# Kernel tuning notes

Hardware: AMD Instinct MI355X
Metric: run time of the kernel (lower is better)

## Reference

```python
import jax, jax.numpy as jnp
import numpy as np

T, H, I, E, TOPK = 2048, 2048, 1408, 8, 2


def setup_inputs() -> dict:
    key = jax.random.key(0)
    k1, k2, k3, k4 = jax.random.split(key, 4)
    x = jax.random.normal(k1, (T, H), dtype=jnp.float32)
    router_logits = jax.random.normal(k2, (T, E), dtype=jnp.float32)
    # scale weights down so activations stay well-conditioned
    w13_weight = jax.random.normal(k3, (E, 2 * I, H), dtype=jnp.float32) * (1.0 / np.sqrt(H))
    w2_weight = jax.random.normal(k4, (E, H, I), dtype=jnp.float32) * (1.0 / np.sqrt(I))
    return {"x": x, "router_logits": router_logits, "w13_weight": w13_weight,
            "w2_weight": w2_weight, "top_k": TOPK}


def reference(x, router_logits, w13_weight, w2_weight, top_k):
    # --- select_experts: softmax scoring, top-k, renormalize ---
    probs = jax.nn.softmax(router_logits.astype(jnp.float32), axis=-1)   # [T, E]
    topk_w, topk_ids = jax.lax.top_k(probs, top_k)                        # [T, k]
    topk_w = topk_w / jnp.sum(topk_w, axis=-1, keepdims=True)             # renormalize
    topk_w = topk_w.astype(x.dtype)

    n_tok = x.shape[0]
    n_exp = w13_weight.shape[0]
    inter = w2_weight.shape[2]

    # dense combine weights [T, E]: zero for unselected experts
    comb = jnp.zeros((n_tok, n_exp), dtype=x.dtype)
    comb = comb.at[jnp.arange(n_tok)[:, None], topk_ids].add(topk_w)

    # --- fused_experts: gated SiLU MLP per expert, weighted combine ---
    gate_up = jnp.einsum('th,eih->tei', x, w13_weight)                    # [T, E, 2I]
    gate, up = gate_up[..., :inter], gate_up[..., inter:]
    act = jax.nn.silu(gate) * up                                          # [T, E, I]
    out = jnp.einsum('tei,ehi,te->th', act, w2_weight, comb)              # [T, H]
    return out
```

## Files before the change

kernel.cpp:

```cpp
#include <hip/hip_runtime.h>
#include <hip/hip_bf16.h>
#include <stdint.h>

#define T_TOK 2048
#define H_DIM 2048
#define I_DIM 1408
#define NEXP  8
#define NPOS  4096
#define NPAD  5120
#define MAXT  40

typedef short short8 __attribute__((ext_vector_type(8)));
typedef float f32x4  __attribute__((ext_vector_type(4)));

__device__ __forceinline__ short f2bf(float f) {
  union { float f; uint32_t u; } v; v.f = f;
  uint32_t r = (v.u + 0x7FFFu + ((v.u >> 16) & 1u)) >> 16;
  return (short)r;
}

__device__ __forceinline__ short8 cvt8(f32x4 a, f32x4 b) {
  __hip_bfloat162 h0 = __float22bfloat162_rn(float2{a[0], a[1]});
  __hip_bfloat162 h1 = __float22bfloat162_rn(float2{a[2], a[3]});
  __hip_bfloat162 h2 = __float22bfloat162_rn(float2{b[0], b[1]});
  __hip_bfloat162 h3 = __float22bfloat162_rn(float2{b[2], b[3]});
  short2 s0, s1, s2, s3;
  __builtin_memcpy(&s0, &h0, 4); __builtin_memcpy(&s1, &h1, 4);
  __builtin_memcpy(&s2, &h2, 4); __builtin_memcpy(&s3, &h3, 4);
  short8 r;
  r[0] = s0.x; r[1] = s0.y; r[2] = s1.x; r[3] = s1.y;
  r[4] = s2.x; r[5] = s2.y; r[6] = s3.x; r[7] = s3.y;
  return r;
}

__device__ __forceinline__ void load_lds16(const void* g, void* l) {
  __builtin_amdgcn_global_load_lds((const __attribute__((address_space(1))) uint32_t*)g,
                                   (__attribute__((address_space(3))) uint32_t*)l,
                                   16, 0, 0);
}

__global__ void k_routing(const float* __restrict__ logits,
                          int* __restrict__ pos_token,
                          float* __restrict__ pos_w,
                          int* __restrict__ eoff,
                          int* __restrict__ inv) {
  __shared__ int   s_ids[T_TOK];
  __shared__ float s_w0[T_TOK];
  __shared__ float s_w1[T_TOK];
  __shared__ int s_cnt[NEXP], s_cur[NEXP], s_off[NEXP + 1];
  const int tid = threadIdx.x;
  if (tid < NEXP) { s_cnt[tid] = 0; s_cur[tid] = 0; }
  for (int p = tid; p < NPAD; p += blockDim.x) { pos_token[p] = 0; pos_w[p] = 0.f; }
  __syncthreads();

  for (int t = tid; t < T_TOK; t += blockDim.x) {
    float l[NEXP];
#pragma unroll
    for (int e = 0; e < NEXP; ++e) l[e] = logits[t * NEXP + e];
    int b0 = 0; float v0 = l[0];
#pragma unroll
    for (int e = 1; e < NEXP; ++e) if (l[e] > v0) { v0 = l[e]; b0 = e; }
    int b1 = -1; float v1 = -1e30f;
#pragma unroll
    for (int e = 0; e < NEXP; ++e) if (e != b0 && l[e] > v1) { v1 = l[e]; b1 = e; }
    float t1 = __expf(v1 - v0);
    float w0 = 1.f / (1.f + t1);
    float w1 = 1.f - w0;
    s_ids[t] = b0 | (b1 << 8);
    s_w0[t] = w0; s_w1[t] = w1;
    atomicAdd(&s_cnt[b0], 1);
    atomicAdd(&s_cnt[b1], 1);
  }
  __syncthreads();
  if (tid == 0) {
    int acc = 0;
    for (int e = 0; e < NEXP; ++e) {
      s_off[e] = acc;
      acc += (s_cnt[e] + 127) & ~127;
    }
    s_off[NEXP] = acc;
    for (int e = 0; e <= NEXP; ++e) eoff[e] = s_off[e];
  }
  __syncthreads();
  for (int t = tid; t < T_TOK; t += blockDim.x) {
    int ids = s_ids[t];
    int e0 = ids & 255, e1 = ids >> 8;
    int p0 = s_off[e0] + atomicAdd(&s_cur[e0], 1);
    pos_token[p0] = t; pos_w[p0] = s_w0[t];
    int p1 = s_off[e1] + atomicAdd(&s_cur[e1], 1);
    pos_token[p1] = t; pos_w[p1] = s_w1[t];
    inv[2 * t] = p0; inv[2 * t + 1] = p1;
  }
}

__global__ void k_gather(const float* __restrict__ x,
                         const int* __restrict__ pos_token,
                         short* __restrict__ xg) {
  const int p = blockIdx.x;
  const int tid = threadIdx.x;
  const int tok = pos_token[p];
  const float4* src = (const float4*)(x + (size_t)tok * H_DIM);
  float4 a = src[tid * 2];
  float4 b = src[tid * 2 + 1];
  short8 s;
  s[0] = f2bf(a.x); s[1] = f2bf(a.y); s[2] = f2bf(a.z); s[3] = f2bf(a.w);
  s[4] = f2bf(b.x); s[5] = f2bf(b.y); s[6] = f2bf(b.z); s[7] = f2bf(b.w);
  ((short8*)(xg + (size_t)p * H_DIM))[tid] = s;
}

__device__ __forceinline__ int tile_expert(const int* eoff, int row0) {
  int e = 0;
#pragma unroll
  for (int i = 1; i < NEXP; ++i) if (row0 >= eoff[i]) e = i;
  return e;
}

__global__ __launch_bounds__(256, 3) void k_gateup(
    const short* __restrict__ xg, const float* __restrict__ w13,
    const int* __restrict__ eoff, short* __restrict__ act) {
  __shared__ __align__(16) short a_s[2][128 * 32];
  __shared__ __align__(16) short bg_s[2][64 * 32];
  __shared__ __align__(16) short bu_s[2][64 * 32];

  int bxr = blockIdx.x;
  const int bx = (bxr & 7) * 110 + (bxr >> 3);
  const int tile = bx / 22;
  const int nt = bx - tile * 22;
  const int row0 = tile * 128;
  if (row0 >= eoff[NEXP]) return;
  const int e = tile_expert(eoff, row0);

  const int tid = threadIdx.x;
  const int wid = tid >> 6;
  const int lane = tid & 63;
  const int wm = wid >> 1, wn = wid & 1;

  f32x4 accg[4][2] = {};
  f32x4 accu[4][2] = {};

  const short* aG  = xg + (size_t)row0 * H_DIM;
  const float* bgG = w13 + (size_t)e * (2 * I_DIM) * H_DIM + (size_t)(nt * 64) * H_DIM;
  const float* buG = bgG + (size_t)I_DIM * H_DIM;

  const int row  = tid >> 2;
  const int scol = ((tid & 3) ^ ((tid >> 3) & 3)) * 8;

  auto stageA = [&](int t, int bi) {
    const int ks = t * 32;
    load_lds16(aG + (size_t)row * H_DIM + ks + scol,        (char*)a_s[bi] + wid * 1024);
    load_lds16(aG + (size_t)(64 + row) * H_DIM + ks + scol, (char*)a_s[bi] + 4096 + wid * 1024);
  };

  f32x4 g0, g1, u0, u1;
  auto ldB = [&](int t) {
    const int ks = t * 32;
    const float* sg = bgG + (size_t)row * H_DIM + ks + scol;
    const float* su = buG + (size_t)row * H_DIM + ks + scol;
    g0 = *(const f32x4*)sg; g1 = *(const f32x4*)(sg + 4);
    u0 = *(const f32x4*)su; u1 = *(const f32x4*)(su + 4);
  };
  auto wrB = [&](int bi) {
    *(short8*)((char*)bg_s[bi] + tid * 16) = cvt8(g0, g1);
    *(short8*)((char*)bu_s[bi] + tid * 16) = cvt8(u0, u1);
  };

  auto compute = [&](int bi) {
    const int asl = ((lane >> 4) ^ ((lane >> 1) & 3)) * 16;
    short8 af[4];
#pragma unroll
    for (int fm = 0; fm < 4; ++fm) {
      int m = wm * 64 + fm * 16 + (lane & 15);
      af[fm] = *(const short8*)((const char*)a_s[bi] + m * 64 + asl);
    }
#pragma unroll
    for (int fn = 0; fn < 2; ++fn) {
      int n = wn * 32 + fn * 16 + (lane & 15);
      short8 bg = *(const short8*)((const char*)bg_s[bi] + n * 64 + asl);
      short8 bu = *(const short8*)((const char*)bu_s[bi] + n * 64 + asl);
#pragma unroll
      for (int fm = 0; fm < 4; ++fm)
        accg[fm][fn] = __builtin_amdgcn_mfma_f32_16x16x32_bf16(af[fm], bg, accg[fm][fn], 0, 0, 0);
#pragma unroll
      for (int fm = 0; fm < 4; ++fm)
        accu[fm][fn] = __builtin_amdgcn_mfma_f32_16x16x32_bf16(af[fm], bu, accu[fm][fn], 0, 0, 0);
    }
  };

  const int NK = H_DIM / 32;
  stageA(0, 0); ldB(0); wrB(0);
  __syncthreads();
  for (int t = 0; t < NK; ++t) {
    int bi = t & 1;
    if (t + 1 < NK) { stageA(t + 1, bi ^ 1); ldB(t + 1); }
    compute(bi);
    if (t + 1 < NK) wrB(bi ^ 1);
    __syncthreads();
  }

#pragma unroll
  for (int fm = 0; fm < 4; ++fm) {
#pragma unroll
    for (int rr = 0; rr < 4; ++rr) {
      int m = wm * 64 + fm * 16 + (lane >> 4) * 4 + rr;
      size_t grow = (size_t)(row0 + m);
#pragma unroll
      for (int fn = 0; fn < 2; ++fn) {
        int col = nt * 64 + wn * 32 + fn * 16 + (lane & 15);
        float g = accg[fm][fn][rr];
        float u = accu[fm][fn][rr];
        float a = g / (1.f + __expf(-g)) * u;
        act[grow * I_DIM + col] = f2bf(a);
      }
    }
  }
}

__global__ __launch_bounds__(256, 3) void k_down(
    const short* __restrict__ act, const float* __restrict__ w2,
    const int* __restrict__ eoff, float* __restrict__ y) {
  __shared__ __align__(16) short a_s[2][128 * 32];
  __shared__ __align__(16) short b_s[2][128 * 32];

  int bxr = blockIdx.x;
  const int bx = (bxr & 7) * 80 + (bxr >> 3);
  const int tile = bx >> 4;
  const int nt = bx & 15;
  const int row0 = tile * 128;
  if (row0 >= eoff[NEXP]) return;
  const int e = tile_expert(eoff, row0);

  const int tid = threadIdx.x;
  const int wid = tid >> 6;
  const int lane = tid & 63;
  const int wm = wid >> 1, wn = wid & 1;

  f32x4 acc[4][4] = {};

  const short* aG = act + (size_t)row0 * I_DIM;
  const float* bG = w2 + (size_t)e * H_DIM * I_DIM + (size_t)(nt * 128) * I_DIM;

  const int row  = tid >> 2;
  const int scol = ((tid & 3) ^ ((tid >> 3) & 3)) * 8;

  auto stageA = [&](int t, int bi) {
    const int ks = t * 32;
    load_lds16(aG + (size_t)row * I_DIM + ks + scol,        (char*)a_s[bi] + wid * 1024);
    load_lds16(aG + (size_t)(64 + row) * I_DIM + ks + scol, (char*)a_s[bi] + 4096 + wid * 1024);
  };

  f32x4 b00, b01, b10, b11;
  auto ldB = [&](int t) {
    const int ks = t * 32;
    const float* s0 = bG + (size_t)row * I_DIM + ks + scol;
    const float* s1 = bG + (size_t)(64 + row) * I_DIM + ks + scol;
    b00 = *(const f32x4*)s0; b01 = *(const f32x4*)(s0 + 4);
    b10 = *(const f32x4*)s1; b11 = *(const f32x4*)(s1 + 4);
  };
  auto wrB = [&](int bi) {
    *(short8*)((char*)b_s[bi] + tid * 16)        = cvt8(b00, b01);
    *(short8*)((char*)b_s[bi] + 4096 + tid * 16) = cvt8(b10, b11);
  };

  auto compute = [&](int bi) {
    const int asl = ((lane >> 4) ^ ((lane >> 1) & 3)) * 16;
    short8 af[4];
#pragma unroll
    for (int fm = 0; fm < 4; ++fm) {
      int m = wm * 64 + fm * 16 + (lane & 15);
      af[fm] = *(const short8*)((const char*)a_s[bi] + m * 64 + asl);
    }
#pragma unroll
    for (int fn = 0; fn < 4; ++fn) {
      int n = wn * 64 + fn * 16 + (lane & 15);
      short8 bb = *(const short8*)((const char*)b_s[bi] + n * 64 + asl);
#pragma unroll
      for (int fm = 0; fm < 4; ++fm)
        acc[fm][fn] = __builtin_amdgcn_mfma_f32_16x16x32_bf16(af[fm], bb, acc[fm][fn], 0, 0, 0);
    }
  };

  const int NK = I_DIM / 32;
  stageA(0, 0); ldB(0); wrB(0);
  __syncthreads();
  for (int t = 0; t < NK; ++t) {
    int bi = t & 1;
    if (t + 1 < NK) { stageA(t + 1, bi ^ 1); ldB(t + 1); }
    compute(bi);
    if (t + 1 < NK) wrB(bi ^ 1);
    __syncthreads();
  }

#pragma unroll
  for (int fm = 0; fm < 4; ++fm) {
#pragma unroll
    for (int rr = 0; rr < 4; ++rr) {
      int m = wm * 64 + fm * 16 + (lane >> 4) * 4 + rr;
      size_t grow = (size_t)(row0 + m);
#pragma unroll
      for (int fn = 0; fn < 4; ++fn) {
        int col = nt * 128 + wn * 64 + fn * 16 + (lane & 15);
        y[grow * H_DIM + col] = acc[fm][fn][rr];
      }
    }
  }
}

__global__ void k_combine(const float* __restrict__ y,
                          const int* __restrict__ inv,
                          const float* __restrict__ pos_w,
                          float* __restrict__ out) {
  const int t = blockIdx.x;
  const int tid = threadIdx.x;
  const int p0 = inv[2 * t], p1 = inv[2 * t + 1];
  const float w0 = pos_w[p0], w1 = pos_w[p1];
  const float4* y0 = (const float4*)(y + (size_t)p0 * H_DIM);
  const float4* y1 = (const float4*)(y + (size_t)p1 * H_DIM);
  float4* o = (float4*)(out + (size_t)t * H_DIM);
#pragma unroll
  for (int i = 0; i < 2; ++i) {
    float4 a = y0[tid * 2 + i];
    float4 b = y1[tid * 2 + i];
    float4 r;
    r.x = w0 * a.x + w1 * b.x;
    r.y = w0 * a.y + w1 * b.y;
    r.z = w0 * a.z + w1 * b.z;
    r.w = w0 * a.w + w1 * b.w;
    o[tid * 2 + i] = r;
  }
}

extern "C" void kernel_launch(void* const* d_in, const int* in_sizes, int n_in,
                              void* d_out, int out_size, void* d_ws, size_t ws_size,
                              hipStream_t stream) {
  const float* x      = (const float*)d_in[0];
  const float* logits = (const float*)d_in[1];
  const float* w13    = (const float*)d_in[2];
  const float* w2     = (const float*)d_in[3];
  (void)in_sizes; (void)n_in; (void)out_size; (void)ws_size;
  float* out = (float*)d_out;
  char* ws = (char*)d_ws;

  size_t o = 0;
  auto alloc = [&](size_t bytes) { size_t r = o; o += (bytes + 255) & ~(size_t)255; return r; };
  short* xg        = (short*)(ws + alloc((size_t)NPAD * H_DIM * 2));
  short* act       = (short*)(ws + alloc((size_t)NPAD * I_DIM * 2));
  float* y         = (float*)(ws + alloc((size_t)NPAD * H_DIM * 4));
  int*   pos_token = (int*)  (ws + alloc((size_t)NPAD * 4));
  float* pos_w     = (float*)(ws + alloc((size_t)NPAD * 4));
  int*   inv       = (int*)  (ws + alloc((size_t)T_TOK * 2 * 4));
  int*   eoff      = (int*)  (ws + alloc((NEXP + 1) * 4));

  k_routing<<<1, 1024, 0, stream>>>(logits, pos_token, pos_w, eoff, inv);
  k_gather<<<NPAD, 256, 0, stream>>>(x, pos_token, xg);
  k_gateup<<<MAXT * 22, 256, 0, stream>>>(xg, w13, eoff, act);
  k_down<<<MAXT * 16, 256, 0, stream>>>(act, w2, eoff, y);
  k_combine<<<T_TOK, 256, 0, stream>>>(y, inv, pos_w, out);
}
```

Measured before the change: 220.2 us.

## Double the expert GEMM row tile to 256 with 512-thread blocks

Pads each expert's token segment to multiples of 256 and doubles the M tile of the gate/up and down GEMMs from 128 to 256 rows. Blocks grow to 512 threads (8 waves), and the weight staging work is split across them. In the gate/up kernel, half the threads stage the gate rows and half stage the up rows. The aim is to halve how often the fp32 expert weights are re-read and converted per token row, at the cost of more padded rows and bigger launches. The gather kernel also switches to the packed bf16 conversion helper.

```diff
diff --git a/kernel.cpp b/kernel.cpp
--- a/kernel.cpp
+++ b/kernel.cpp
@@ -5,10 +5,11 @@
 #define T_TOK 2048
 #define H_DIM 2048
 #define I_DIM 1408
+#define GU_W  2816
 #define NEXP  8
 #define NPOS  4096
-#define NPAD  5120
-#define MAXT  40
+#define NPAD  6144
+#define T256  24
 
 typedef short short8 __attribute__((ext_vector_type(8)));
 typedef float f32x4  __attribute__((ext_vector_type(4)));
@@ -76,7 +77,7 @@
     int acc = 0;
     for (int e = 0; e < NEXP; ++e) {
       s_off[e] = acc;
-      acc += (s_cnt[e] + 127) & ~127;
+      acc += (s_cnt[e] + 255) & ~255;
     }
     s_off[NEXP] = acc;
     for (int e = 0; e <= NEXP; ++e) eoff[e] = s_off[e];
@@ -99,13 +100,10 @@
   const int p = blockIdx.x;
   const int tid = threadIdx.x;
   const int tok = pos_token[p];
-  const float4* src = (const float4*)(x + (size_t)tok * H_DIM);
-  float4 a = src[tid * 2];
-  float4 b = src[tid * 2 + 1];
-  short8 s;
-  s[0] = f2bf(a.x); s[1] = f2bf(a.y); s[2] = f2bf(a.z); s[3] = f2bf(a.w);
-  s[4] = f2bf(b.x); s[5] = f2bf(b.y); s[6] = f2bf(b.z); s[7] = f2bf(b.w);
-  ((short8*)(xg + (size_t)p * H_DIM))[tid] = s;
+  const f32x4* src = (const f32x4*)(x + (size_t)tok * H_DIM);
+  f32x4 a = src[tid * 2];
+  f32x4 b = src[tid * 2 + 1];
+  ((short8*)(xg + (size_t)p * H_DIM))[tid] = cvt8(a, b);
 }
 
 __device__ __forceinline__ int tile_expert(const int* eoff, int row0) {
@@ -115,18 +113,18 @@
   return e;
 }
 
-__global__ __launch_bounds__(256, 3) void k_gateup(
+__global__ __launch_bounds__(512, 4) void k_gateup(
     const short* __restrict__ xg, const float* __restrict__ w13,
     const int* __restrict__ eoff, short* __restrict__ act) {
-  __shared__ __align__(16) short a_s[2][128 * 32];
+  __shared__ __align__(16) short a_s[2][256 * 32];
   __shared__ __align__(16) short bg_s[2][64 * 32];
   __shared__ __align__(16) short bu_s[2][64 * 32];
 
   int bxr = blockIdx.x;
-  const int bx = (bxr & 7) * 110 + (bxr >> 3);
+  const int bx = (bxr & 7) * 66 + (bxr >> 3);
   const int tile = bx / 22;
   const int nt = bx - tile * 22;
-  const int row0 = tile * 128;
+  const int row0 = tile * 256;
   if (row0 >= eoff[NEXP]) return;
   const int e = tile_expert(eoff, row0);
 
@@ -139,29 +137,30 @@
   f32x4 accu[4][2] = {};
 
   const short* aG  = xg + (size_t)row0 * H_DIM;
-  const float* bgG = w13 + (size_t)e * (2 * I_DIM) * H_DIM + (size_t)(nt * 64) * H_DIM;
+  const float* bgG = w13 + (size_t)e * GU_W * H_DIM + (size_t)(nt * 64) * H_DIM;
   const float* buG = bgG + (size_t)I_DIM * H_DIM;
 
   const int row  = tid >> 2;
   const int scol = ((tid & 3) ^ ((tid >> 3) & 3)) * 8;
+  const int t2   = tid & 255;
+  const int brow = t2 >> 2;
+  const int bscol = ((t2 & 3) ^ ((t2 >> 3) & 3)) * 8;
+  const float* bHalf = (tid < 256) ? bgG : buG;
 
   auto stageA = [&](int t, int bi) {
     const int ks = t * 32;
-    load_lds16(aG + (size_t)row * H_DIM + ks + scol,        (char*)a_s[bi] + wid * 1024);
-    load_lds16(aG + (size_t)(64 + row) * H_DIM + ks + scol, (char*)a_s[bi] + 4096 + wid * 1024);
-  };
-
-  f32x4 g0, g1, u0, u1;
+    load_lds16(aG + (size_t)row * H_DIM + ks + scol,         (char*)a_s[bi] + wid * 1024);
+    load_lds16(aG + (size_t)(128 + row) * H_DIM + ks + scol, (char*)a_s[bi] + 8192 + wid * 1024);
+  };
+  f32x4 b0, b1;
   auto ldB = [&](int t) {
     const int ks = t * 32;
-    const float* sg = bgG + (size_t)row * H_DIM + ks + scol;
-    const float* su = buG + (size_t)row * H_DIM + ks + scol;
-    g0 = *(const f32x4*)sg; g1 = *(const f32x4*)(sg + 4);
-    u0 = *(const f32x4*)su; u1 = *(const f32x4*)(su + 4);
+    const float* s = bHalf + (size_t)brow * H_DIM + ks + bscol;
+    b0 = *(const f32x4*)s; b1 = *(const f32x4*)(s + 4);
   };
   auto wrB = [&](int bi) {
-    *(short8*)((char*)bg_s[bi] + tid * 16) = cvt8(g0, g1);
-    *(short8*)((char*)bu_s[bi] + tid * 16) = cvt8(u0, u1);
+    char* d = (tid < 256) ? (char*)bg_s[bi] : (char*)bu_s[bi];
+    *(short8*)(d + t2 * 16) = cvt8(b0, b1);
   };
 
   auto compute = [&](int bi) {
@@ -215,17 +214,17 @@
   }
 }
 
-__global__ __launch_bounds__(256, 3) void k_down(
+__global__ __launch_bounds__(512, 4) void k_down(
     const short* __restrict__ act, const float* __restrict__ w2,
     const int* __restrict__ eoff, float* __restrict__ y) {
-  __shared__ __align__(16) short a_s[2][128 * 32];
+  __shared__ __align__(16) short a_s[2][256 * 32];
   __shared__ __align__(16) short b_s[2][128 * 32];
 
   int bxr = blockIdx.x;
-  const int bx = (bxr & 7) * 80 + (bxr >> 3);
+  const int bx = (bxr & 7) * 48 + (bxr >> 3);
   const int tile = bx >> 4;
   const int nt = bx & 15;
-  const int row0 = tile * 128;
+  const int row0 = tile * 256;
   if (row0 >= eoff[NEXP]) return;
   const int e = tile_expert(eoff, row0);
 
@@ -244,21 +243,17 @@
 
   auto stageA = [&](int t, int bi) {
     const int ks = t * 32;
-    load_lds16(aG + (size_t)row * I_DIM + ks + scol,        (char*)a_s[bi] + wid * 1024);
-    load_lds16(aG + (size_t)(64 + row) * I_DIM + ks + scol, (char*)a_s[bi] + 4096 + wid * 1024);
-  };
-
-  f32x4 b00, b01, b10, b11;
+    load_lds16(aG + (size_t)row * I_DIM + ks + scol,         (char*)a_s[bi] + wid * 1024);
+    load_lds16(aG + (size_t)(128 + row) * I_DIM + ks + scol, (char*)a_s[bi] + 8192 + wid * 1024);
+  };
+  f32x4 b0, b1;
   auto ldB = [&](int t) {
     const int ks = t * 32;
-    const float* s0 = bG + (size_t)row * I_DIM + ks + scol;
-    const float* s1 = bG + (size_t)(64 + row) * I_DIM + ks + scol;
-    b00 = *(const f32x4*)s0; b01 = *(const f32x4*)(s0 + 4);
-    b10 = *(const f32x4*)s1; b11 = *(const f32x4*)(s1 + 4);
+    const float* s = bG + (size_t)row * I_DIM + ks + scol;
+    b0 = *(const f32x4*)s; b1 = *(const f32x4*)(s + 4);
   };
   auto wrB = [&](int bi) {
-    *(short8*)((char*)b_s[bi] + tid * 16)        = cvt8(b00, b01);
-    *(short8*)((char*)b_s[bi] + 4096 + tid * 16) = cvt8(b10, b11);
+    *(short8*)((char*)b_s[bi] + tid * 16) = cvt8(b0, b1);
   };
 
   auto compute = [&](int bi) {
@@ -352,7 +347,7 @@
 
   k_routing<<<1, 1024, 0, stream>>>(logits, pos_token, pos_w, eoff, inv);
   k_gather<<<NPAD, 256, 0, stream>>>(x, pos_token, xg);
-  k_gateup<<<MAXT * 22, 256, 0, stream>>>(xg, w13, eoff, act);
-  k_down<<<MAXT * 16, 256, 0, stream>>>(act, w2, eoff, y);
+  k_gateup<<<T256 * 22, 512, 0, stream>>>(xg, w13, eoff, act);
+  k_down<<<T256 * 16, 512, 0, stream>>>(act, w2, eoff, y);
   k_combine<<<T_TOK, 256, 0, stream>>>(y, inv, pos_w, out);
 }
```

Measured after the change: 242.0 us. +9.9%, slower.
